# Kernel optimization log

Hardware: AMD Instinct MI355X
Metric: run time of the kernel (lower is better)

## Reference

```python
import jax, jax.numpy as jnp
import numpy as np

D_MODEL = 1024
NUM_HEADS = 16
HEAD_DIM = D_MODEL // NUM_HEADS


def setup_inputs() -> dict:
    key = jax.random.key(0)
    ks = jax.random.split(key, 11)
    B, S = 2, 2048
    s = 1.0 / np.sqrt(D_MODEL)
    inp = {
        'q': jax.random.normal(ks[0], (B, S, D_MODEL), jnp.float32),
        'k': jax.random.normal(ks[1], (B, S, D_MODEL), jnp.float32),
        'v': jax.random.normal(ks[2], (B, S, D_MODEL), jnp.float32),
        'wq': jax.random.normal(ks[3], (D_MODEL, D_MODEL), jnp.float32) * s,
        'bq': jnp.zeros((D_MODEL,), jnp.float32),
        'wk': jax.random.normal(ks[4], (D_MODEL, D_MODEL), jnp.float32) * s,
        'bk': jnp.zeros((D_MODEL,), jnp.float32),
        'wv': jax.random.normal(ks[5], (D_MODEL, D_MODEL), jnp.float32) * s,
        'bv': jnp.zeros((D_MODEL,), jnp.float32),
        'wo': jax.random.normal(ks[6], (D_MODEL, D_MODEL), jnp.float32) * s,
        'bo': jnp.zeros((D_MODEL,), jnp.float32),
    }
    return inp


def _split_heads(x, B):
    # [B, S, D] -> [B, H, S, Hd]
    return x.reshape(B, -1, NUM_HEADS, HEAD_DIM).transpose(0, 2, 1, 3)


def reference(q, k, v, wq, bq, wk, bk, wv, bv, wo, bo):
    B = q.shape[0]
    qh = _split_heads(q @ wq + bq, B)
    kh = _split_heads(k @ wk + bk, B)
    vh = _split_heads(v @ wv + bv, B)
    scale = 1.0 / np.sqrt(HEAD_DIM).astype(np.float32)
    # [B, H, Sq, Sk]
    scores = jnp.einsum('bhqd,bhkd->bhqk', qh, kh) * scale
    probs = jax.nn.softmax(scores, axis=-1)
    out = jnp.einsum('bhqk,bhkd->bhqd', probs, vh)  # [B, H, Sq, Hd]
    out = out.transpose(0, 2, 1, 3).reshape(B, -1, D_MODEL)
    return out @ wo + bo
```

## Files before the change

### kernel.cpp

```cpp
#include <hip/hip_runtime.h>

typedef unsigned short u16;
typedef __bf16 bf16x8 __attribute__((ext_vector_type(8)));
typedef float    f32x4 __attribute__((ext_vector_type(4)));
typedef float   f32x16 __attribute__((ext_vector_type(16)));
typedef u16      u16x8 __attribute__((ext_vector_type(8)));
typedef u16      u16x4 __attribute__((ext_vector_type(4)));
typedef unsigned uint4v __attribute__((ext_vector_type(4)));

#define DM 1024
#define SQ 2048
#define HD 64
#define QSCALE 0.18033688f

#define SWZ8(row, ch) ((((ch) ^ ((row) & 7) ^ ((row) >> 3)) & 7))

__device__ __forceinline__ u16 f2bf(float f) {
    unsigned u = __builtin_bit_cast(unsigned, f);
    u += 0x7FFFu + ((u >> 16) & 1u);
    return (u16)(u >> 16);
}

__device__ __forceinline__ bf16x8 ldsbf(const u16* p) {
    return __builtin_bit_cast(bf16x8, *(const u16x8*)p);
}

__device__ __forceinline__ unsigned cvtpk(float a, float b) {
    unsigned r;
    asm("v_cvt_pk_bf16_f32 %0, %1, %2" : "=v"(r) : "v"(a), "v"(b));
    return r;
}

__device__ __forceinline__ void swap32(unsigned &a, unsigned &b) {
    asm volatile("v_permlane32_swap_b32 %0, %1" : "+v"(a), "+v"(b));
}

typedef __attribute__((address_space(3))) unsigned lds_u32_t;
typedef __attribute__((address_space(1))) const unsigned glob_u32_t;
__device__ __forceinline__ void gl_lds16(const u16* g, u16* l) {
    __builtin_amdgcn_global_load_lds((glob_u32_t*)g, (lds_u32_t*)l, 16, 0, 0);
}

__global__ __launch_bounds__(256) void wtrans_kernel(
    const float* __restrict__ w0, const float* __restrict__ w1,
    const float* __restrict__ w2, const float* __restrict__ w3,
    u16* __restrict__ t0, u16* __restrict__ t1,
    u16* __restrict__ t2, u16* __restrict__ t3)
{
    __shared__ float tile[32][33];
    const int z = blockIdx.z;
    const float* W = (z==0) ? w0 : (z==1) ? w1 : (z==2) ? w2 : w3;
    u16* T        = (z==0) ? t0 : (z==1) ? t1 : (z==2) ? t2 : t3;
    const float sc = (z==0) ? QSCALE : 1.0f;
    const int tx = threadIdx.x & 31, ty = threadIdx.x >> 5;
    const int n0 = blockIdx.x * 32, k0 = blockIdx.y * 32;
#pragma unroll
    for (int i = 0; i < 4; ++i)
        tile[ty + 8*i][tx] = W[(size_t)(k0 + ty + 8*i)*DM + n0 + tx];
    __syncthreads();
#pragma unroll
    for (int i = 0; i < 4; ++i)
        T[(size_t)(n0 + ty + 8*i)*DM + k0 + tx] = f2bf(tile[tx][ty + 8*i] * sc);
}

template<bool AFP32, bool OF32, bool VTLAST>
__global__ __launch_bounds__(256) void gemm_kernel(
    const void* __restrict__ a0, const void* __restrict__ a1, const void* __restrict__ a2,
    const u16* __restrict__ w0, const u16* __restrict__ w1, const u16* __restrict__ w2,
    const float* __restrict__ bi0, const float* __restrict__ bi1, const float* __restrict__ bi2,
    void* __restrict__ o0, void* __restrict__ o1, void* __restrict__ o2,
    float bscale0)
{
    __shared__ __align__(16) u16 As[128*64];
    __shared__ __align__(16) u16 Bs[128*64];

    const int cpx  = gridDim.x >> 3;
    const int wgid = (blockIdx.x & 7) * cpx + (blockIdx.x >> 3);
    const int z   = wgid >> 8;
    const int rem = wgid & 255;
    const int by  = rem >> 3, bx = rem & 7;

    const void* Ap  = (z==0) ? a0 : (z==1) ? a1 : a2;
    const u16*  Wp  = (z==0) ? w0 : (z==1) ? w1 : w2;
    const float* Bp = (z==0) ? bi0 : (z==1) ? bi1 : bi2;
    void* Op        = (z==0) ? o0 : (z==1) ? o1 : o2;
    const float bsc = (z==0) ? bscale0 : 1.0f;

    const int tid  = threadIdx.x;
    const int lane = tid & 63;
    const int wv   = tid >> 6;
    const int m0 = by * 128;
    const int n0 = bx * 128;
    const int wr = (wv >> 1) * 64;
    const int wc = (wv & 1) * 64;
    const int g  = lane >> 4;
    const int mm = lane & 15;

    const int l8  = lane >> 3;
    const int chs = (lane & 7) ^ l8;
    const int lrow = wv*8 + l8;
    const int srow = tid >> 3;
    const int c8   = tid & 7;

    const f32x4 zero4 = {0.f, 0.f, 0.f, 0.f};
    f32x4 acc[4][4];
#pragma unroll
    for (int i = 0; i < 4; ++i)
#pragma unroll
        for (int j = 0; j < 4; ++j) acc[i][j] = zero4;

    for (int kt = 0; kt < 16; ++kt) {
        const int k0 = kt * 64;
#pragma unroll
        for (int i = 0; i < 4; ++i) {
            const int row = i*32 + lrow;
            gl_lds16(&Wp[(size_t)(n0+row)*DM + k0 + chs*8], &Bs[(i*32 + wv*8)*64]);
        }
        if (AFP32) {
#pragma unroll
            for (int p = 0; p < 4; ++p) {
                const int row = p*32 + srow;
                const float* src = (const float*)Ap + (size_t)(m0+row)*DM + k0 + c8*8;
                f32x4 x0 = *(const f32x4*)src;
                f32x4 x1 = *(const f32x4*)(src + 4);
                uint4v w;
                w[0] = cvtpk(x0[0], x0[1]);
                w[1] = cvtpk(x0[2], x0[3]);
                w[2] = cvtpk(x1[0], x1[1]);
                w[3] = cvtpk(x1[2], x1[3]);
                *(uint4v*)&As[row*64 + ((c8 ^ (row & 7)) << 3)] = w;
            }
        } else {
#pragma unroll
            for (int i = 0; i < 4; ++i) {
                const int row = i*32 + lrow;
                gl_lds16(&((const u16*)Ap)[(size_t)(m0+row)*DM + k0 + chs*8],
                         &As[(i*32 + wv*8)*64]);
            }
        }
        __syncthreads();
#pragma unroll
        for (int ks = 0; ks < 2; ++ks) {
            bf16x8 af[4], bfr[4];
#pragma unroll
            for (int rt = 0; rt < 4; ++rt) {
                const int row = wr + rt*16 + mm;
                const int ch  = ks*4 + g;
                af[rt] = ldsbf(&As[row*64 + ((ch ^ (row & 7)) << 3)]);
            }
#pragma unroll
            for (int ct = 0; ct < 4; ++ct) {
                const int row = wc + ct*16 + mm;
                const int ch  = ks*4 + g;
                bfr[ct] = ldsbf(&Bs[row*64 + ((ch ^ (row & 7)) << 3)]);
            }
            __builtin_amdgcn_s_setprio(1);
#pragma unroll
            for (int rt = 0; rt < 4; ++rt)
#pragma unroll
                for (int ct = 0; ct < 4; ++ct)
                    acc[rt][ct] = __builtin_amdgcn_mfma_f32_16x16x32_bf16(
                        af[rt], bfr[ct], acc[rt][ct], 0, 0, 0);
            __builtin_amdgcn_s_setprio(0);
        }
        __syncthreads();
    }
    if (VTLAST && z == 2) {
#pragma unroll
        for (int ct = 0; ct < 4; ++ct) {
            const int col = n0 + wc + ct*16 + mm;
            const float bv = Bp[col] * bsc;
#pragma unroll
            for (int rt = 0; rt < 4; ++rt) {
                const int row0 = m0 + wr + rt*16 + g*4;
                const int bb = row0 >> 11, s = row0 & (SQ-1);
                u16x4 pk;
#pragma unroll
                for (int r = 0; r < 4; ++r) pk[r] = f2bf(acc[rt][ct][r] + bv);
                *(u16x4*)&((u16*)Op)[(size_t)(bb*DM + col)*SQ + s] = pk;
            }
        }
    } else {
#pragma unroll
        for (int ct = 0; ct < 4; ++ct) {
            const int col = n0 + wc + ct*16 + mm;
            const float bv = Bp[col] * bsc;
#pragma unroll
            for (int rt = 0; rt < 4; ++rt) {
#pragma unroll
                for (int r = 0; r < 4; ++r) {
                    const int row = m0 + wr + rt*16 + g*4 + r;
                    const float vv = acc[rt][ct][r] + bv;
                    if (OF32) ((float*)Op)[(size_t)row*DM + col] = vv;
                    else      ((u16*) Op)[(size_t)row*DM + col] = f2bf(vv);
                }
            }
        }
    }
}

__global__ __launch_bounds__(512) void attn_kernel(
    const u16* __restrict__ Q, const u16* __restrict__ K,
    const u16* __restrict__ Vt, u16* __restrict__ Z)
{
    __shared__ __align__(16) u16 Kl[2][64*64];
    __shared__ __align__(16) u16 Vl[2][64*64];

    const int tid  = threadIdx.x;
    const int lane = tid & 63;
    const int wid  = tid >> 6;
    const int c    = lane & 31;
    const int hi   = lane >> 5;
    const int srow = tid >> 3;
    const int c8   = tid & 7;

    const int wg = (blockIdx.x & 7) * 32 + (blockIdx.x >> 3);
    const int qt = wg & 7;
    const int hb = wg >> 3;
    const int h  = hb & 15;
    const int b  = hb >> 4;
    const int q0 = qt * 256;

    const size_t kbase = (size_t)(b*SQ)*DM + h*HD;
    const size_t vbase = (size_t)((b*16 + h)*HD)*SQ;

    bf16x8 qf[4];
    {
        const size_t qoff = (size_t)(b*SQ + q0 + wid*32 + c)*DM + h*HD + hi*8;
#pragma unroll
        for (int ks = 0; ks < 4; ++ks)
            qf[ks] = ldsbf(&Q[qoff + ks*16]);
    }

    f32x16 oacc[2];
#pragma unroll
    for (int dt = 0; dt < 2; ++dt)
#pragma unroll
        for (int r = 0; r < 16; ++r) oacc[dt][r] = 0.f;
    f32x16 z16;
#pragma unroll
    for (int r = 0; r < 16; ++r) z16[r] = 0.f;
    float lsp[4] = {0.f, 0.f, 0.f, 0.f};

    const int stw = srow*64 + (SWZ8(srow, c8) << 3);
    u16x8 kreg = *(const u16x8*)&K [kbase + (size_t)srow*DM + c8*8];
    u16x8 vreg = *(const u16x8*)&Vt[vbase + (size_t)srow*SQ + c8*8];
    *(u16x8*)&Kl[0][stw] = kreg;
    *(u16x8*)&Vl[0][stw] = vreg;

    for (int t = 0; t < SQ/64; ++t) {
        const int cur = t & 1;
        __syncthreads();
        if (t + 1 < SQ/64) {
            kreg = *(const u16x8*)&K [kbase + (size_t)((t+1)*64 + srow)*DM + c8*8];
            vreg = *(const u16x8*)&Vt[vbase + (size_t)srow*SQ + (t+1)*64 + c8*8];
        }

        f32x16 pacc[2];
        __builtin_amdgcn_s_setprio(1);
#pragma unroll
        for (int kt = 0; kt < 2; ++kt) {
            const int row = kt*32 + c;
            bf16x8 kf = ldsbf(&Kl[cur][row*64 + (SWZ8(row, hi) << 3)]);
            pacc[kt] = __builtin_amdgcn_mfma_f32_32x32x16_bf16(kf, qf[0], z16, 0, 0, 0);
        }
#pragma unroll
        for (int ks = 1; ks < 4; ++ks) {
#pragma unroll
            for (int kt = 0; kt < 2; ++kt) {
                const int row = kt*32 + c;
                const int ch  = ks*2 + hi;
                bf16x8 kf = ldsbf(&Kl[cur][row*64 + (SWZ8(row, ch) << 3)]);
                pacc[kt] = __builtin_amdgcn_mfma_f32_32x32x16_bf16(kf, qf[ks], pacc[kt], 0, 0, 0);
            }
        }
        __builtin_amdgcn_s_setprio(0);

#pragma unroll
        for (int kt = 0; kt < 2; ++kt)
#pragma unroll
            for (int r = 0; r < 16; ++r) {
                const float e = __builtin_amdgcn_exp2f(pacc[kt][r]);
                pacc[kt][r] = e;
                lsp[r & 3] += e;
            }

        bf16x8 pa[4];
#pragma unroll
        for (int kt = 0; kt < 2; ++kt)
#pragma unroll
            for (int k2 = 0; k2 < 2; ++k2) {
                const int bs = k2*8;
                unsigned u = cvtpk(pacc[kt][bs+0], pacc[kt][bs+1]);
                unsigned v = cvtpk(pacc[kt][bs+2], pacc[kt][bs+3]);
                unsigned w = cvtpk(pacc[kt][bs+4], pacc[kt][bs+5]);
                unsigned x = cvtpk(pacc[kt][bs+6], pacc[kt][bs+7]);
                swap32(u, w);
                swap32(v, x);
                uint4v fr = {u, v, w, x};
                pa[kt*2 + k2] = __builtin_bit_cast(bf16x8, fr);
            }

        __builtin_amdgcn_s_setprio(1);
#pragma unroll
        for (int kp = 0; kp < 4; ++kp) {
#pragma unroll
            for (int dt = 0; dt < 2; ++dt) {
                const int d  = dt*32 + c;
                const int ch = kp*2 + hi;
                bf16x8 vf = ldsbf(&Vl[cur][d*64 + (SWZ8(d, ch) << 3)]);
                oacc[dt] = __builtin_amdgcn_mfma_f32_32x32x16_bf16(pa[kp], vf, oacc[dt], 0, 0, 0);
            }
        }
        __builtin_amdgcn_s_setprio(0);

        if (t + 1 < SQ/64) {
            *(u16x8*)&Kl[cur^1][stw] = kreg;
            *(u16x8*)&Vl[cur^1][stw] = vreg;
        }
    }

    float lsum = (lsp[0] + lsp[1]) + (lsp[2] + lsp[3]);
    lsum += __shfl_xor(lsum, 32, 64);
    const float linv = 1.f / lsum;
    float linvr[16];
#pragma unroll
    for (int r = 0; r < 16; ++r)
        linvr[r] = __shfl(linv, (r & 3) + 8*(r >> 2) + 4*hi, 64);

#pragma unroll
    for (int dt = 0; dt < 2; ++dt)
#pragma unroll
        for (int r = 0; r < 16; ++r) {
            const int qrl = (r & 3) + 8*(r >> 2) + 4*hi;
            const size_t row = (size_t)(b*SQ + q0 + wid*32 + qrl);
            Z[row*DM + h*HD + dt*32 + c] = f2bf(oacc[dt][r] * linvr[r]);
        }
}

extern "C" void kernel_launch(void* const* d_in, const int* in_sizes, int n_in,
                              void* d_out, int out_size, void* d_ws, size_t ws_size,
                              hipStream_t stream)
{
    const float* q  = (const float*)d_in[0];
    const float* k  = (const float*)d_in[1];
    const float* v  = (const float*)d_in[2];
    const float* wq = (const float*)d_in[3];
    const float* bq = (const float*)d_in[4];
    const float* wk = (const float*)d_in[5];
    const float* bk = (const float*)d_in[6];
    const float* wv = (const float*)d_in[7];
    const float* bv = (const float*)d_in[8];
    const float* wo = (const float*)d_in[9];
    const float* bo = (const float*)d_in[10];
    float* out = (float*)d_out;

    char* ws = (char*)d_ws;
    u16* Qb  = (u16*)(ws);
    u16* Kb  = (u16*)(ws + 8388608);
    u16* VtB = (u16*)(ws + 16777216);
    u16* Zb  = (u16*)(ws + 25165824);
    u16* WtQ = (u16*)(ws + 33554432);
    u16* WtK = (u16*)(ws + 35651584);
    u16* WtV = (u16*)(ws + 37748736);
    u16* WtO = (u16*)(ws + 39845888);

    wtrans_kernel<<<dim3(32, 32, 4), 256, 0, stream>>>(
        wq, wk, wv, wo, WtQ, WtK, WtV, WtO);

    gemm_kernel<true, false, true><<<dim3(768), 256, 0, stream>>>(
        (const void*)q, (const void*)k, (const void*)v,
        WtQ, WtK, WtV, bq, bk, bv,
        (void*)Qb, (void*)Kb, (void*)VtB, QSCALE);

    attn_kernel<<<dim3(256), 512, 0, stream>>>(Qb, Kb, VtB, Zb);

    gemm_kernel<false, true, false><<<dim3(256), 256, 0, stream>>>(
        (const void*)Zb, (const void*)Zb, (const void*)Zb,
        WtO, WtO, WtO, bo, bo, bo,
        (void*)out, (void*)out, (void*)out, 1.0f);
}
```

Measured before the change: 123.9 us.

## Double-buffer LDS tiles in projection GEMM to overlap loads with MFMA

The projection GEMM now uses two LDS buffers for the A and W tiles. The next k-tile is prefetched while MFMAs run on the current one: direct global-to-LDS loads for W and bf16 A, and register staging followed by a late convert-and-write for fp32 A. This removes one barrier per iteration and hides global-load latency. In exchange, LDS use per block doubles to 64 KB, which may reduce occupancy, and the held fp32 registers raise register pressure.

```diff
diff --git a/kernel.cpp b/kernel.cpp
--- a/kernel.cpp
+++ b/kernel.cpp
@@ -71,8 +71,8 @@
     void* __restrict__ o0, void* __restrict__ o1, void* __restrict__ o2,
     float bscale0)
 {
-    __shared__ __align__(16) u16 As[128*64];
-    __shared__ __align__(16) u16 Bs[128*64];
+    __shared__ __align__(16) u16 As[2][128*64];
+    __shared__ __align__(16) u16 Bs[2][128*64];
 
     const int cpx  = gridDim.x >> 3;
     const int wgid = (blockIdx.x & 7) * cpx + (blockIdx.x >> 3);
@@ -102,6 +102,8 @@
     const int srow = tid >> 3;
     const int c8   = tid & 7;
 
+    f32x4 ar[4][2];
+
     const f32x4 zero4 = {0.f, 0.f, 0.f, 0.f};
     f32x4 acc[4][4];
 #pragma unroll
@@ -109,36 +111,56 @@
 #pragma unroll
         for (int j = 0; j < 4; ++j) acc[i][j] = zero4;
 
-    for (int kt = 0; kt < 16; ++kt) {
-        const int k0 = kt * 64;
+    auto stageW = [&](int kt, int buf) {
 #pragma unroll
         for (int i = 0; i < 4; ++i) {
             const int row = i*32 + lrow;
-            gl_lds16(&Wp[(size_t)(n0+row)*DM + k0 + chs*8], &Bs[(i*32 + wv*8)*64]);
-        }
-        if (AFP32) {
-#pragma unroll
-            for (int p = 0; p < 4; ++p) {
-                const int row = p*32 + srow;
-                const float* src = (const float*)Ap + (size_t)(m0+row)*DM + k0 + c8*8;
-                f32x4 x0 = *(const f32x4*)src;
-                f32x4 x1 = *(const f32x4*)(src + 4);
-                uint4v w;
-                w[0] = cvtpk(x0[0], x0[1]);
-                w[1] = cvtpk(x0[2], x0[3]);
-                w[2] = cvtpk(x1[0], x1[1]);
-                w[3] = cvtpk(x1[2], x1[3]);
-                *(uint4v*)&As[row*64 + ((c8 ^ (row & 7)) << 3)] = w;
-            }
-        } else {
-#pragma unroll
-            for (int i = 0; i < 4; ++i) {
-                const int row = i*32 + lrow;
-                gl_lds16(&((const u16*)Ap)[(size_t)(m0+row)*DM + k0 + chs*8],
-                         &As[(i*32 + wv*8)*64]);
-            }
-        }
-        __syncthreads();
+            gl_lds16(&Wp[(size_t)(n0+row)*DM + kt*64 + chs*8],
+                     &Bs[buf][(i*32 + wv*8)*64]);
+        }
+    };
+    auto stageA_lds = [&](int kt, int buf) {
+#pragma unroll
+        for (int i = 0; i < 4; ++i) {
+            const int row = i*32 + lrow;
+            gl_lds16(&((const u16*)Ap)[(size_t)(m0+row)*DM + kt*64 + chs*8],
+                     &As[buf][(i*32 + wv*8)*64]);
+        }
+    };
+    auto loadA = [&](int kt) {
+#pragma unroll
+        for (int p = 0; p < 4; ++p) {
+            const int row = p*32 + srow;
+            const float* src = (const float*)Ap + (size_t)(m0+row)*DM + kt*64 + c8*8;
+            ar[p][0] = *(const f32x4*)src;
+            ar[p][1] = *(const f32x4*)(src + 4);
+        }
+    };
+    auto writeA = [&](int buf) {
+#pragma unroll
+        for (int p = 0; p < 4; ++p) {
+            const int row = p*32 + srow;
+            uint4v w;
+            w[0] = cvtpk(ar[p][0][0], ar[p][0][1]);
+            w[1] = cvtpk(ar[p][0][2], ar[p][0][3]);
+            w[2] = cvtpk(ar[p][1][0], ar[p][1][1]);
+            w[3] = cvtpk(ar[p][1][2], ar[p][1][3]);
+            *(uint4v*)&As[buf][row*64 + ((c8 ^ (row & 7)) << 3)] = w;
+        }
+    };
+
+    stageW(0, 0);
+    if (AFP32) { loadA(0); writeA(0); }
+    else       stageA_lds(0, 0);
+    __syncthreads();
+
+    for (int kt = 0; kt < 16; ++kt) {
+        const int cur = kt & 1;
+        if (kt < 15) {
+            stageW(kt + 1, cur ^ 1);
+            if (AFP32) loadA(kt + 1);
+            else       stageA_lds(kt + 1, cur ^ 1);
+        }
 #pragma unroll
         for (int ks = 0; ks < 2; ++ks) {
             bf16x8 af[4], bfr[4];
@@ -146,13 +168,13 @@
             for (int rt = 0; rt < 4; ++rt) {
                 const int row = wr + rt*16 + mm;
                 const int ch  = ks*4 + g;
-                af[rt] = ldsbf(&As[row*64 + ((ch ^ (row & 7)) << 3)]);
+                af[rt] = ldsbf(&As[cur][row*64 + ((ch ^ (row & 7)) << 3)]);
             }
 #pragma unroll
             for (int ct = 0; ct < 4; ++ct) {
                 const int row = wc + ct*16 + mm;
                 const int ch  = ks*4 + g;
-                bfr[ct] = ldsbf(&Bs[row*64 + ((ch ^ (row & 7)) << 3)]);
+                bfr[ct] = ldsbf(&Bs[cur][row*64 + ((ch ^ (row & 7)) << 3)]);
             }
             __builtin_amdgcn_s_setprio(1);
 #pragma unroll
@@ -163,8 +185,12 @@
                         af[rt], bfr[ct], acc[rt][ct], 0, 0, 0);
             __builtin_amdgcn_s_setprio(0);
         }
-        __syncthreads();
+        if (kt < 15) {
+            if (AFP32) writeA(cur ^ 1);
+            __syncthreads();
+        }
     }
+
     if (VTLAST && z == 2) {
 #pragma unroll
         for (int ct = 0; ct < 4; ++ct) {
```

New measurement: 118.7 us. 4.2% less time.
